# Optimization experiments

Measured on AMD Instinct MI355X. Metric: run time of the kernel, lower is better.

## Reference

```python
import jax, jax.numpy as jnp
import numpy as np

SAMPLE_RATE = 16000
LOW_CUTOFF = 3400.0   # max(cutoff_freq) -> lowpass stage
HIGH_CUTOFF = 300.0   # min(cutoff_freq) -> highpass stage
Q = 0.7071067811865476  # torchaudio default Q = 1/sqrt(2)


def _lowpass_coeffs(cutoff, sr):
    w0 = 2.0 * np.pi * cutoff / sr
    alpha = np.sin(w0) / (2.0 * Q)
    cw = np.cos(w0)
    b0 = (1.0 - cw) / 2.0
    b1 = 1.0 - cw
    b2 = b0
    a0 = 1.0 + alpha
    a1 = -2.0 * cw
    a2 = 1.0 - alpha
    return tuple(np.float32(c / a0) for c in (b0, b1, b2, a1, a2))


def _highpass_coeffs(cutoff, sr):
    w0 = 2.0 * np.pi * cutoff / sr
    alpha = np.sin(w0) / (2.0 * Q)
    cw = np.cos(w0)
    b0 = (1.0 + cw) / 2.0
    b1 = -(1.0 + cw)
    b2 = b0
    a0 = 1.0 + alpha
    a1 = -2.0 * cw
    a2 = 1.0 - alpha
    return tuple(np.float32(c / a0) for c in (b0, b1, b2, a1, a2))


def _biquad(x, coeffs):
    """Direct-form-II-transposed biquad along the last (time) axis.
    x: [B, C, T]. Matches torchaudio lfilter with a0-normalized coeffs,
    followed by the torchaudio default clamp to [-1, 1]."""
    b0, b1, b2, a1, a2 = (jnp.asarray(c, x.dtype) for c in coeffs)
    xt = jnp.moveaxis(x, -1, 0)  # [T, B, C] for time scan

    def step(carry, xi):
        s1, s2 = carry
        y = b0 * xi + s1
        s1n = b1 * xi - a1 * y + s2
        s2n = b2 * xi - a2 * y
        return (s1n, s2n), y

    zeros = jnp.zeros(x.shape[:-1], x.dtype)
    _, yt = jax.lax.scan(step, (zeros, zeros), xt)
    y = jnp.moveaxis(yt, 0, -1)  # back to [B, C, T]
    return jnp.clip(y, -1.0, 1.0)


def setup_inputs() -> dict:
    key = jax.random.key(0)
    # scale down so the post-filter clamp to [-1,1] rarely saturates (audio-like amplitudes)
    waveform = 0.1 * jax.random.normal(key, (32, 2, 480000), dtype=jnp.float32)
    return {"waveform": waveform}


def reference(waveform):
    # bandpass = lowpass(max cutoff) then highpass(min cutoff)
    y = _biquad(waveform, _lowpass_coeffs(LOW_CUTOFF, SAMPLE_RATE))
    y = _biquad(y, _highpass_coeffs(HIGH_CUTOFF, SAMPLE_RATE))
    return y
```

## Files before the change

kernel.cpp:

```cpp
#include <hip/hip_runtime.h>
#include <math.h>


#define NT    128
#define LCH   32
#define WUC   4
#define CH_F4 9
#define NCH   NT
#define OUTC  (NT - WUC)
#define SPAN  (OUTC * LCH)
#define T_LEN 480000

struct ScanConsts {
    float p[7][16];
    float e[LCH][4];
    float h[LCH];
    float kk[LCH][4];
};

#define PCOMB(P_, prev, val) {                                                                                \
        float4 nv;                                                                                            \
        nv.x = fmaf((P_)[ 0], prev.x, fmaf((P_)[ 1], prev.y, fmaf((P_)[ 2], prev.z, fmaf((P_)[ 3], prev.w, val.x)))); \
        nv.y = fmaf((P_)[ 4], prev.x, fmaf((P_)[ 5], prev.y, fmaf((P_)[ 6], prev.z, fmaf((P_)[ 7], prev.w, val.y)))); \
        nv.z = fmaf((P_)[ 8], prev.x, fmaf((P_)[ 9], prev.y, fmaf((P_)[10], prev.z, fmaf((P_)[11], prev.w, val.z)))); \
        nv.w = fmaf((P_)[12], prev.x, fmaf((P_)[13], prev.y, fmaf((P_)[14], prev.z, fmaf((P_)[15], prev.w, val.w)))); \
        val = nv;                                                                                             \
    }

#define PMATV(P_, v) {                                                                     \
        float4 nv;                                                                         \
        nv.x = fmaf((P_)[ 0], v.x, fmaf((P_)[ 1], v.y, fmaf((P_)[ 2], v.z, (P_)[ 3]*v.w))); \
        nv.y = fmaf((P_)[ 4], v.x, fmaf((P_)[ 5], v.y, fmaf((P_)[ 6], v.z, (P_)[ 7]*v.w))); \
        nv.z = fmaf((P_)[ 8], v.x, fmaf((P_)[ 9], v.y, fmaf((P_)[10], v.z, (P_)[11]*v.w))); \
        nv.w = fmaf((P_)[12], v.x, fmaf((P_)[13], v.y, fmaf((P_)[14], v.z, (P_)[15]*v.w))); \
        v = nv;                                                                            \
    }

__global__ __launch_bounds__(NT, 4)
void bandpass_kernel(const float* __restrict__ in, float* __restrict__ out,
                     ScanConsts SC) {
    __shared__ float4 lds4[NCH * CH_F4];
    const int tid  = threadIdx.x;
    const int lane = tid & 63;
    const long tile_start = (long)blockIdx.x * SPAN;
    const float* __restrict__ src = in  + (long)blockIdx.y * T_LEN;
    float*       __restrict__ dst = out + (long)blockIdx.y * T_LEN;

    #pragma unroll
    for (int it = 0; it < 8; ++it) {
        int k = tid + it * NT;
        long g = tile_start - (WUC * LCH) + 4L * k;
        float4 v = make_float4(0.f, 0.f, 0.f, 0.f);
        if (g >= 0 && g + 4 <= T_LEN) v = *(const float4*)(src + g);
        lds4[CH_F4 * (k >> 3) + (k & 7)] = v;
    }
    __syncthreads();

    float xs[LCH];
    {
        const float4* cp = &lds4[CH_F4 * tid];
        #pragma unroll
        for (int q = 0; q < 8; ++q) {
            float4 v = cp[q];
            xs[4*q+0] = v.x; xs[4*q+1] = v.y; xs[4*q+2] = v.z; xs[4*q+3] = v.w;
        }
    }

    float4 val = make_float4(0.f, 0.f, 0.f, 0.f);
    #pragma unroll
    for (int j = 0; j < LCH; ++j) {
        const float* K = SC.kk[j];
        val.x = fmaf(K[0], xs[j], val.x);
        val.y = fmaf(K[1], xs[j], val.y);
        val.z = fmaf(K[2], xs[j], val.z);
        val.w = fmaf(K[3], xs[j], val.w);
    }

    #pragma unroll
    for (int k = 0; k < 6; ++k) {
        const int off = 1 << k;
        float4 prev;
        prev.x = __shfl_up(val.x, off);
        prev.y = __shfl_up(val.y, off);
        prev.z = __shfl_up(val.z, off);
        prev.w = __shfl_up(val.w, off);
        if (lane >= off) {
            const float* P_ = SC.p[k];
            PCOMB(P_, prev, val);
        }
    }
    if (tid == 63) lds4[CH_F4 * 63 + 8] = val;
    __syncthreads();
    if (tid >= 64) {
        float4 v = lds4[CH_F4 * 63 + 8];
        const int n = lane + 1;
        #pragma unroll
        for (int k = 0; k < 7; ++k) {
            if ((n >> k) & 1) { const float* P_ = SC.p[k]; PMATV(P_, v); }
        }
        val.x += v.x; val.y += v.y; val.z += v.z; val.w += v.w;
    }
    float4 s0;
    s0.x = __shfl_up(val.x, 1);
    s0.y = __shfl_up(val.y, 1);
    s0.z = __shfl_up(val.z, 1);
    s0.w = __shfl_up(val.w, 1);
    if (tid == 0)  s0 = make_float4(0.f, 0.f, 0.f, 0.f);
    if (tid == 64) s0 = lds4[CH_F4 * 63 + 8];

#define CONV1(i, dst_) {                                                              \
        const float* E = SC.e[i];                                                     \
        float acc = fmaf(E[0], s0.x, fmaf(E[1], s0.y, fmaf(E[2], s0.z, E[3]*s0.w)));  \
        _Pragma("unroll")                                                             \
        for (int j = 0; j <= (i); ++j) acc = fmaf(SC.h[(i)-j], xs[j], acc);           \
        dst_ = fminf(fmaxf(acc, -1.f), 1.f);                                          \
    }
    {
        float4* mp = &lds4[CH_F4 * tid];
        #pragma unroll
        for (int q = 0; q < 8; ++q) {
            float4 r;
            CONV1(4*q+0, r.x);
            CONV1(4*q+1, r.y);
            CONV1(4*q+2, r.z);
            CONV1(4*q+3, r.w);
            mp[q] = r;
        }
    }
#undef CONV1
    __syncthreads();

    for (int k = tid; k < SPAN / 4; k += NT) {
        long g = tile_start + 4L * k;
        if (g + 4 <= T_LEN) {
            *(float4*)(dst + g) = lds4[CH_F4 * ((k >> 3) + WUC) + (k & 7)];
        }
    }
}
#undef PCOMB
#undef PMATV

static void biquad_coeffs_d(double cutoff, double sr, bool highpass, double* c) {
    const double Q  = 0.7071067811865476;
    const double w0 = 2.0 * M_PI * cutoff / sr;
    const double al = sin(w0) / (2.0 * Q);
    const double cw = cos(w0);
    double b0, b1, b2;
    if (highpass) { b0 = (1.0 + cw) / 2.0; b1 = -(1.0 + cw); b2 = b0; }
    else          { b0 = (1.0 - cw) / 2.0; b1 =  (1.0 - cw); b2 = b0; }
    const double a0 = 1.0 + al;
    c[0] = b0 / a0;
    c[1] = b1 / a0;
    c[2] = b2 / a0;
    c[3] = -(-2.0 * cw) / a0;
    c[4] = -(1.0 - al) / a0;
}

static void matmul4(const double* A, const double* B, double* C) {
    for (int r = 0; r < 4; ++r)
        for (int c = 0; c < 4; ++c) {
            double s = 0.0;
            for (int k = 0; k < 4; ++k) s += A[r * 4 + k] * B[k * 4 + c];
            C[r * 4 + c] = s;
        }
}

extern "C" void kernel_launch(void* const* d_in, const int* in_sizes, int n_in,
                              void* d_out, int out_size, void* d_ws, size_t ws_size,
                              hipStream_t stream) {
    const float* in  = (const float*)d_in[0];
    float*       out = (float*)d_out;

    double lpd[5], hpd[5];
    biquad_coeffs_d(3400.0, 16000.0, false, lpd);
    biquad_coeffs_d(300.0, 16000.0, true, hpd);

    ScanConsts SC;

    double M[16];
    for (int j = 0; j < 4; ++j) {
        double s1a = (j == 0), s2a = (j == 1), s1b = (j == 2), s2b = (j == 3);
        double y1  = s1a;
        double n1a = lpd[3] * y1 + s2a;
        double n2a = lpd[4] * y1;
        double y2  = hpd[0] * y1 + s1b;
        double n1b = hpd[1] * y1 + hpd[3] * y2 + s2b;
        double n2b = hpd[2] * y1 + hpd[4] * y2;
        M[0 * 4 + j] = n1a;
        M[1 * 4 + j] = n2a;
        M[2 * 4 + j] = n1b;
        M[3 * 4 + j] = n2b;
    }

    double A[16], T[16];
    for (int i = 0; i < 16; ++i) A[i] = M[i];
    for (int s = 0; s < 5; ++s) { matmul4(A, A, T); for (int i = 0; i < 16; ++i) A[i] = T[i]; }
    double Pk[16];
    for (int i = 0; i < 16; ++i) Pk[i] = A[i];
    for (int k = 0; k < 7; ++k) {
        for (int i = 0; i < 16; ++i) SC.p[k][i] = (float)Pk[i];
        matmul4(Pk, Pk, T);
        for (int i = 0; i < 16; ++i) Pk[i] = T[i];
    }

    for (int j = 0; j < 4; ++j) {
        double s1a = (j == 0), s2a = (j == 1), s1b = (j == 2), s2b = (j == 3);
        for (int i = 0; i < LCH; ++i) {
            double y1  = s1a;
            double n1a = lpd[3] * y1 + s2a;
            double n2a = lpd[4] * y1;
            double y2  = hpd[0] * y1 + s1b;
            double n1b = hpd[1] * y1 + hpd[3] * y2 + s2b;
            double n2b = hpd[2] * y1 + hpd[4] * y2;
            SC.e[i][j] = (float)y2;
            s1a = n1a; s2a = n2a; s1b = n1b; s2b = n2b;
        }
    }

    {
        double s1a = 0, s2a = 0, s1b = 0, s2b = 0;
        double Sarr[LCH][4];
        for (int n = 0; n < LCH; ++n) {
            double x   = (n == 0) ? 1.0 : 0.0;
            double y1  = lpd[0] * x + s1a;
            double n1a = lpd[1] * x + lpd[3] * y1 + s2a;
            double n2a = lpd[2] * x + lpd[4] * y1;
            double x2  = y1;
            double y2  = hpd[0] * x2 + s1b;
            double n1b = hpd[1] * x2 + hpd[3] * y2 + s2b;
            double n2b = hpd[2] * x2 + hpd[4] * y2;
            SC.h[n] = (float)y2;
            s1a = n1a; s2a = n2a; s1b = n1b; s2b = n2b;
            Sarr[n][0] = s1a; Sarr[n][1] = s2a; Sarr[n][2] = s1b; Sarr[n][3] = s2b;
        }
        for (int j = 0; j < LCH; ++j)
            for (int c = 0; c < 4; ++c)
                SC.kk[j][c] = (float)Sarr[LCH - 1 - j][c];
    }

    const int n_seq  = in_sizes[0] / T_LEN;
    const int n_tile = (T_LEN + SPAN - 1) / SPAN;

    dim3 grid(n_tile, n_seq);
    bandpass_kernel<<<grid, NT, 0, stream>>>(in, out, SC);
}
```

Before: 226.3 us.

## Make each wavefront an independent tile, dropping LDS staging and cross-wave scan

Each 64-lane wavefront now handles its own tile of 60 output chunks plus 4 warm-up chunks. Lanes load their 32 samples straight from global memory and write outputs straight back. This removes the LDS staging buffer, all __syncthreads barriers and the second-level cross-wave prefix combine, so one fewer scan matrix is needed. In exchange, warm-up recomputation rises from 4 of 128 chunks to 4 of 64, and global accesses become lane-strided by 128 bytes instead of coalesced. The launch becomes a 1-D grid of 256-thread blocks, with the launch-bounds hint raised to 8.

Measured after the change: 348.1 us. +53.8%, slower.

```diff
diff --git a/kernel.cpp b/kernel.cpp
--- a/kernel.cpp
+++ b/kernel.cpp
@@ -2,17 +2,18 @@
 #include <math.h>
 
 
-#define NT    128
 #define LCH   32
 #define WUC   4
-#define CH_F4 9
-#define NCH   NT
-#define OUTC  (NT - WUC)
+#define CPW   64
+#define OUTC  (CPW - WUC)
 #define SPAN  (OUTC * LCH)
 #define T_LEN 480000
+#define TILES (T_LEN / SPAN)
+#define NT    256
+#define WPB   (NT / 64)
 
 struct ScanConsts {
-    float p[7][16];
+    float p[6][16];
     float e[LCH][4];
     float h[LCH];
     float kk[LCH][4];
@@ -27,43 +28,29 @@
         val = nv;                                                                                             \
     }
 
-#define PMATV(P_, v) {                                                                     \
-        float4 nv;                                                                         \
-        nv.x = fmaf((P_)[ 0], v.x, fmaf((P_)[ 1], v.y, fmaf((P_)[ 2], v.z, (P_)[ 3]*v.w))); \
-        nv.y = fmaf((P_)[ 4], v.x, fmaf((P_)[ 5], v.y, fmaf((P_)[ 6], v.z, (P_)[ 7]*v.w))); \
-        nv.z = fmaf((P_)[ 8], v.x, fmaf((P_)[ 9], v.y, fmaf((P_)[10], v.z, (P_)[11]*v.w))); \
-        nv.w = fmaf((P_)[12], v.x, fmaf((P_)[13], v.y, fmaf((P_)[14], v.z, (P_)[15]*v.w))); \
-        v = nv;                                                                            \
-    }
-
-__global__ __launch_bounds__(NT, 4)
+__global__ __launch_bounds__(NT, 8)
 void bandpass_kernel(const float* __restrict__ in, float* __restrict__ out,
                      ScanConsts SC) {
-    __shared__ float4 lds4[NCH * CH_F4];
-    const int tid  = threadIdx.x;
-    const int lane = tid & 63;
-    const long tile_start = (long)blockIdx.x * SPAN;
-    const float* __restrict__ src = in  + (long)blockIdx.y * T_LEN;
-    float*       __restrict__ dst = out + (long)blockIdx.y * T_LEN;
-
-    #pragma unroll
-    for (int it = 0; it < 8; ++it) {
-        int k = tid + it * NT;
-        long g = tile_start - (WUC * LCH) + 4L * k;
-        float4 v = make_float4(0.f, 0.f, 0.f, 0.f);
-        if (g >= 0 && g + 4 <= T_LEN) v = *(const float4*)(src + g);
-        lds4[CH_F4 * (k >> 3) + (k & 7)] = v;
-    }
-    __syncthreads();
+    const int lane    = threadIdx.x & 63;
+    const int wave_id = blockIdx.x * WPB + (threadIdx.x >> 6);
+    const int seq     = wave_id / TILES;
+    const int tile    = wave_id - seq * TILES;
+    const float* __restrict__ src = in  + (long)seq * T_LEN;
+    float*       __restrict__ dst = out + (long)seq * T_LEN;
+
+    const long base = (long)tile * SPAN + ((long)lane - WUC) * LCH;
 
     float xs[LCH];
-    {
-        const float4* cp = &lds4[CH_F4 * tid];
+    if (base >= 0) {
+        const float4* p4 = (const float4*)(src + base);
         #pragma unroll
         for (int q = 0; q < 8; ++q) {
-            float4 v = cp[q];
+            float4 v = p4[q];
             xs[4*q+0] = v.x; xs[4*q+1] = v.y; xs[4*q+2] = v.z; xs[4*q+3] = v.w;
         }
+    } else {
+        #pragma unroll
+        for (int i = 0; i < LCH; ++i) xs[i] = 0.f;
     }
 
     float4 val = make_float4(0.f, 0.f, 0.f, 0.f);
@@ -89,24 +76,12 @@
             PCOMB(P_, prev, val);
         }
     }
-    if (tid == 63) lds4[CH_F4 * 63 + 8] = val;
-    __syncthreads();
-    if (tid >= 64) {
-        float4 v = lds4[CH_F4 * 63 + 8];
-        const int n = lane + 1;
-        #pragma unroll
-        for (int k = 0; k < 7; ++k) {
-            if ((n >> k) & 1) { const float* P_ = SC.p[k]; PMATV(P_, v); }
-        }
-        val.x += v.x; val.y += v.y; val.z += v.z; val.w += v.w;
-    }
     float4 s0;
     s0.x = __shfl_up(val.x, 1);
     s0.y = __shfl_up(val.y, 1);
     s0.z = __shfl_up(val.z, 1);
     s0.w = __shfl_up(val.w, 1);
-    if (tid == 0)  s0 = make_float4(0.f, 0.f, 0.f, 0.f);
-    if (tid == 64) s0 = lds4[CH_F4 * 63 + 8];
+    if (lane == 0) s0 = make_float4(0.f, 0.f, 0.f, 0.f);
 
 #define CONV1(i, dst_) {                                                              \
         const float* E = SC.e[i];                                                     \
@@ -115,8 +90,8 @@
         for (int j = 0; j <= (i); ++j) acc = fmaf(SC.h[(i)-j], xs[j], acc);           \
         dst_ = fminf(fmaxf(acc, -1.f), 1.f);                                          \
     }
-    {
-        float4* mp = &lds4[CH_F4 * tid];
+    if (lane >= WUC) {
+        float4* p4 = (float4*)(dst + base);
         #pragma unroll
         for (int q = 0; q < 8; ++q) {
             float4 r;
@@ -124,21 +99,12 @@
             CONV1(4*q+1, r.y);
             CONV1(4*q+2, r.z);
             CONV1(4*q+3, r.w);
-            mp[q] = r;
+            p4[q] = r;
         }
     }
 #undef CONV1
-    __syncthreads();
-
-    for (int k = tid; k < SPAN / 4; k += NT) {
-        long g = tile_start + 4L * k;
-        if (g + 4 <= T_LEN) {
-            *(float4*)(dst + g) = lds4[CH_F4 * ((k >> 3) + WUC) + (k & 7)];
-        }
-    }
 }
 #undef PCOMB
-#undef PMATV
 
 static void biquad_coeffs_d(double cutoff, double sr, bool highpass, double* c) {
     const double Q  = 0.7071067811865476;
@@ -197,7 +163,7 @@
     for (int s = 0; s < 5; ++s) { matmul4(A, A, T); for (int i = 0; i < 16; ++i) A[i] = T[i]; }
     double Pk[16];
     for (int i = 0; i < 16; ++i) Pk[i] = A[i];
-    for (int k = 0; k < 7; ++k) {
+    for (int k = 0; k < 6; ++k) {
         for (int i = 0; i < 16; ++i) SC.p[k][i] = (float)Pk[i];
         matmul4(Pk, Pk, T);
         for (int i = 0; i < 16; ++i) Pk[i] = T[i];
@@ -238,9 +204,9 @@
                 SC.kk[j][c] = (float)Sarr[LCH - 1 - j][c];
     }
 
-    const int n_seq  = in_sizes[0] / T_LEN;
-    const int n_tile = (T_LEN + SPAN - 1) / SPAN;
-
-    dim3 grid(n_tile, n_seq);
-    bandpass_kernel<<<grid, NT, 0, stream>>>(in, out, SC);
-}
+    const int n_seq   = in_sizes[0] / T_LEN;
+    const int n_waves = n_seq * TILES;
+    const int n_blk   = n_waves / WPB;
+
+    bandpass_kernel<<<dim3(n_blk), NT, 0, stream>>>(in, out, SC);
+}
```
